# Optimization experiments

Measured on AMD Instinct MI355X. Metric: run time of the kernel, lower is better.

## Reference

```python
import jax, jax.numpy as jnp
import numpy as np

H, W, C = 96, 96, 21
SIGMA_RGB = 3.0   # bilateral spatial sdims (as called in the original code)
SIGMA_XY = 64.0   # gaussian spatial sdims
SCHAN = 255.0     # bilateral color std
COMPAT = 10.0     # Potts compatibility weight (same for both kernels)
N_ITERS = 5


def _gauss_kernel(feats):
    # feats: [N, D] -> K[i,j] = exp(-0.5 * ||f_i - f_j||^2)
    sq = jnp.sum(feats * feats, axis=-1)
    d2 = sq[:, None] + sq[None, :] - 2.0 * (feats @ feats.T)
    return jnp.exp(-0.5 * jnp.maximum(d2, 0.0))


def setup_inputs() -> dict:
    key = jax.random.key(0)
    k1, k2, k3 = jax.random.split(key, 3)
    logits = jax.random.normal(k1, (1, C, H, W), dtype=jnp.float32)
    labels = jax.random.randint(k2, (1, H, W), 0, C, dtype=jnp.int32)
    image = jax.random.uniform(k3, (1, 3, H, W), dtype=jnp.float32) * 255.0
    return {"logits": logits, "labels": labels, "image": image, "num_classes": C}


def reference(logits, labels, image, num_classes):
    # unary potentials: U = -log_softmax(logits)
    logp = jax.nn.log_softmax(logits, axis=1)              # [1,C,H,W]
    U = (-logp)[0].reshape(num_classes, -1).T              # [N,C]

    # pixel features
    yy, xx = jnp.meshgrid(jnp.arange(H), jnp.arange(W), indexing="ij")
    pos = jnp.stack([yy, xx], axis=-1).reshape(-1, 2).astype(logits.dtype)  # [N,2]
    rgb = image[0].transpose(1, 2, 0).reshape(-1, 3)        # [N,3]

    # dense pairwise kernels (exact Gaussian / bilateral, self-connection removed)
    N = H * W
    eye = jnp.eye(N, dtype=logits.dtype)
    Kg = _gauss_kernel(pos / SIGMA_XY) - eye
    fb = jnp.concatenate([pos / SIGMA_RGB, rgb / SCHAN], axis=-1)
    Kb = _gauss_kernel(fb) - eye

    # mean-field inference, Potts compatibility mu(l,l') = [l != l']
    Q0 = jax.nn.softmax(-U, axis=1)                         # [N,C]

    def step(Q, _):
        msg = Kg @ Q + Kb @ Q                               # [N,C] filtered Q
        pair = COMPAT * (jnp.sum(msg, axis=1, keepdims=True) - msg)
        Q = jax.nn.softmax(-U - pair, axis=1)
        return Q, None

    Q, _ = jax.lax.scan(step, Q0, None, length=N_ITERS)
    pairwise = Q.T.reshape(1, num_classes, H, W)

    # cross entropy (mean over pixels)
    ce = -jnp.mean(jnp.take_along_axis(logp, labels[:, None].astype(jnp.int32), axis=1))

    return ce + pairwise                                    # broadcast, as in original
```

## Files before the change

kernel.cpp:

```cpp
#include <hip/hip_runtime.h>
#include <hip/hip_fp16.h>

#define HH 96
#define WW 96
#define CC 21
#define NN (HH*WW)
#define NBLK (NN/256)
#define STRIDE 24
#define ROWF (WW*STRIDE)
#define QTROWS 24

typedef _Float16 f16x8 __attribute__((ext_vector_type(8)));
typedef float f32x4 __attribute__((ext_vector_type(4)));

union H8 { f16x8 v; __half2 h2[4]; };


__global__ __launch_bounds__(256) void k_setup(
    const float* __restrict__ logits, const int* __restrict__ labels,
    const float* __restrict__ image, float* __restrict__ U,
    float* __restrict__ Q0, _Float16* __restrict__ QTa,
    _Float16* __restrict__ QTb, float* __restrict__ gtab,
    float* __restrict__ partial) {
  const int t = threadIdx.x;
  const int i = blockIdx.x * 256 + t;

  float d[CC];
  float mx = -1e30f;
#pragma unroll
  for (int c = 0; c < CC; ++c) {
    d[c] = logits[c * NN + i];
    mx = fmaxf(mx, d[c]);
  }
  float s = 0.f;
#pragma unroll
  for (int c = 0; c < CC; ++c) { d[c] -= mx; s += __expf(d[c]); }
  const float lse = logf(s);
  const float inv = 1.f / s;
  const int lab = labels[i];
  float myU = 0.f;
#pragma unroll
  for (int c = 0; c < CC; ++c) {
    const float Uc = lse - d[c];
    const float q = __expf(d[c]) * inv;
    U[i * STRIDE + c] = Uc;
    Q0[i * STRIDE + c] = q;
    QTa[c * NN + i] = (_Float16)q;
    myU = (c == lab) ? Uc : myU;
  }
  const float rr = image[i] * (1.f / 255.f);
  const float rg = image[NN + i] * (1.f / 255.f);
  const float rb = image[2 * NN + i] * (1.f / 255.f);
  U[i * STRIDE + 21] = 0.f;
  U[i * STRIDE + 22] = 0.f;
  U[i * STRIDE + 23] = 0.f;
  Q0[i * STRIDE + 21] = rr;
  Q0[i * STRIDE + 22] = rg;
  Q0[i * STRIDE + 23] = rb;
  QTa[21 * NN + i] = (_Float16)rr;
  QTa[22 * NN + i] = (_Float16)rg;
  QTa[23 * NN + i] = (_Float16)rb;
  QTb[21 * NN + i] = (_Float16)rr;
  QTb[22 * NN + i] = (_Float16)rg;
  QTb[23 * NN + i] = (_Float16)rb;

  if (blockIdx.x == 0 && t < 96) {
    const float dv = (float)t * (1.f / 64.f);
    gtab[t] = __expf(-0.5f * dv * dv);
  }

  __shared__ float red[256];
  red[t] = myU;
  __syncthreads();
  for (int off = 128; off > 0; off >>= 1) {
    if (t < off) red[t] += red[t + off];
    __syncthreads();
  }
  if (t == 0) partial[blockIdx.x] = red[0];
}

__global__ __launch_bounds__(256) void k_gauss_y(
    const float* __restrict__ Qin, float* __restrict__ Gy,
    const float* __restrict__ gtab) {
  __shared__ float g[96];
  if (threadIdx.x < 96) g[threadIdx.x] = gtab[threadIdx.x];
  __syncthreads();
  const int idx = blockIdx.x * 256 + threadIdx.x;
  const int y = idx / ROWF;
  const int rem = idx - y * ROWF;
  const float* base = Qin + rem;
  float acc = 0.f;
#pragma unroll 8
  for (int yp = 0; yp < HH; ++yp)
    acc = fmaf(g[abs(y - yp)], base[yp * ROWF], acc);
  Gy[idx] = acc;
}

__global__ __launch_bounds__(256) void k_gauss_x(
    const float* __restrict__ Gy, float* __restrict__ G,
    const float* __restrict__ gtab) {
  __shared__ float g[96];
  if (threadIdx.x < 96) g[threadIdx.x] = gtab[threadIdx.x];
  __syncthreads();
  const int idx = blockIdx.x * 256 + threadIdx.x;
  const int y = idx / ROWF;
  const int rem = idx - y * ROWF;
  const int x = rem / STRIDE;
  const int c = rem - x * STRIDE;
  const float* base = Gy + y * ROWF + c;
  float acc = 0.f;
#pragma unroll 8
  for (int xp = 0; xp < WW; ++xp)
    acc = fmaf(g[abs(x - xp)], base[xp * STRIDE], acc);
  G[idx] = acc;
}

__global__ __launch_bounds__(512) void k_bilat(
    const float* __restrict__ U, const float* __restrict__ Qin,
    const float* __restrict__ G, const _Float16* __restrict__ QT,
    float* __restrict__ Qout, _Float16* __restrict__ QTout) {
  __shared__ __half sytab[64];
  __shared__ __half2 sxtab[64];
  __shared__ float psum[8][16][24];

  const int tid = threadIdx.x;
  const int w = tid >> 6;
  const int l = tid & 63;
  const int g = l >> 4;
  const int q = l & 15;

  if (tid < 64) {
    const float dv = (float)(tid - 32);
    sytab[tid] = __float2half(__expf(dv * dv * (-1.f / 18.f)));
    const float dv1 = dv + 1.f;
    sxtab[tid] = __floats2half2_rn(__expf(dv * dv * (-1.f / 18.f)),
                                   __expf(dv1 * dv1 * (-1.f / 18.f)));
  }
  __syncthreads();

  const int tile = blockIdx.x;
  const int ty0 = (tile / 24) * 4;
  const int tx0 = (tile - (tile / 24) * 24) * 4;

  const int pr = q >> 2, pc = q & 3;
  const int yi = ty0 + pr, xi = tx0 + pc;
  const int ipix = yi * WW + xi;

  const float4 rown = *(const float4*)(Qin + ipix * STRIDE + 20);
  const __half2 ri_r = __float2half2_rn(rown.y);
  const __half2 ri_g = __float2half2_rn(rown.z);
  const __half2 ri_b = __float2half2_rn(rown.w);
  const __half2 mhalf = __floats2half2_rn(-0.5f, -0.5f);
  const __half hzero = __float2half(0.f);

  const int xs = tx0 - 16;
  const int xbase0 = (xs > 0 ? xs : 0) & ~7;
  const int rows0 = (w < 4) ? w * 5 : 20 + (w - 4) * 4;
  const int nrun = ((w < 4) ? 5 : 4) * 5;
  const int nck = (nrun + 3) >> 2;

  const int brow2 = (16 + q > 23) ? 23 : 16 + q;

  f32x4 acc0 = {0.f, 0.f, 0.f, 0.f};
  f32x4 acc1 = {0.f, 0.f, 0.f, 0.f};

#pragma unroll 2
  for (int ck = 0; ck < 7; ++ck) {
    if (ck >= nck) break;
    const int r = ck * 4 + g;
    const int wr = r / 5;
    const int cs = r - wr * 5;
    const int yj = ty0 - 16 + rows0 + wr;
    const int xb = xbase0 + cs * 8;
    const bool ok = (r < nrun) & (yj >= 0) & (yj < HH) & (xb <= WW - 8);
    const int yc = min(max(yj, 0), HH - 1);
    const int xc = min(xb, WW - 8);
    const int jb = yc * WW + xc;

    H8 b1, b2, rj, gj, bj;
    b1.v = *(const f16x8*)(QT + q * NN + jb);
    b2.v = *(const f16x8*)(QT + brow2 * NN + jb);
    rj.v = *(const f16x8*)(QT + 21 * NN + jb);
    gj.v = *(const f16x8*)(QT + 22 * NN + jb);
    bj.v = *(const f16x8*)(QT + 23 * NN + jb);

    const int dy = yj - yi;
    const int iy = min(max(dy + 32, 0), 63);
    const __half syv = ok ? sytab[iy] : hzero;
    const __half2 sy2 = __half2half2(syv);
    const int dx0 = xb - xi;
    const int ix0 = min(max(dx0 + 32, 0), 57);

    H8 af;
#pragma unroll
    for (int e2 = 0; e2 < 4; ++e2) {
      const __half2 sx2 = sxtab[ix0 + 2 * e2];
      const __half2 dr = __hsub2(rj.h2[e2], ri_r);
      const __half2 dg = __hsub2(gj.h2[e2], ri_g);
      const __half2 db = __hsub2(bj.h2[e2], ri_b);
      __half2 d2c = __hmul2(dr, dr);
      d2c = __hfma2(dg, dg, d2c);
      d2c = __hfma2(db, db, d2c);
      const __half2 ec = h2exp(__hmul2(d2c, mhalf));
      af.h2[e2] = __hmul2(__hmul2(sy2, sx2), ec);
    }
    acc0 = __builtin_amdgcn_mfma_f32_16x16x32_f16(af.v, b1.v, acc0, 0, 0, 0);
    acc1 = __builtin_amdgcn_mfma_f32_16x16x32_f16(af.v, b2.v, acc1, 0, 0, 0);
  }

#pragma unroll
  for (int reg = 0; reg < 4; ++reg) {
    psum[w][g * 4 + reg][q] = acc0[reg];
    if (q < 8) psum[w][g * 4 + reg][16 + q] = acc1[reg];
  }
  __syncthreads();

  const int half_ = l >> 5;
  const int cl = l & 31;
  const bool act = cl < CC;
  const int pix = w * 2 + half_;
  const int ip = (ty0 + (pix >> 2)) * WW + tx0 + (pix & 3);
  float Qic = 0.f;
  if (cl < STRIDE) Qic = Qin[ip * STRIDE + cl];
  float tcv = 0.f, Uc = 0.f, Gc = 0.f;
  if (act) {
    tcv = psum[0][pix][cl] + psum[1][pix][cl] + psum[2][pix][cl] +
          psum[3][pix][cl] + psum[4][pix][cl] + psum[5][pix][cl] +
          psum[6][pix][cl] + psum[7][pix][cl];
    Uc = U[ip * STRIDE + cl];
    Gc = G[ip * STRIDE + cl];
  }
  const float contrib = act ? (tcv + Gc - 2.f * Qic) : 0.f;
  float tot = contrib;
#pragma unroll
  for (int off = 16; off >= 1; off >>= 1) tot += __shfl_xor(tot, off, 32);
  const float lc = act ? (-Uc - 10.f * (tot - contrib)) : -1e30f;
  float mxl = lc;
#pragma unroll
  for (int off = 16; off >= 1; off >>= 1)
    mxl = fmaxf(mxl, __shfl_xor(mxl, off, 32));
  const float e = act ? __expf(lc - mxl) : 0.f;
  float se = e;
#pragma unroll
  for (int off = 16; off >= 1; off >>= 1) se += __shfl_xor(se, off, 32);
  const float qnew = e / se;
  if (cl < STRIDE) Qout[ip * STRIDE + cl] = act ? qnew : Qic;
  if (act) QTout[cl * NN + ip] = (_Float16)qnew;
}

__global__ __launch_bounds__(256) void k_out(
    const float* __restrict__ Q, const float* __restrict__ partial,
    float* __restrict__ out) {
  __shared__ float ces;
  if (threadIdx.x < 64) {
    float v = (threadIdx.x < NBLK) ? partial[threadIdx.x] : 0.f;
#pragma unroll
    for (int off = 32; off > 0; off >>= 1) v += __shfl_down(v, off);
    if (threadIdx.x == 0) ces = v * (1.f / (float)NN);
  }
  __syncthreads();
  const int idx = blockIdx.x * 256 + threadIdx.x;
  if (idx >= CC * NN) return;
  const int c = idx / NN;
  const int i = idx - c * NN;
  out[idx] = ces + Q[i * STRIDE + c];
}

extern "C" void kernel_launch(void* const* d_in, const int* in_sizes, int n_in,
                              void* d_out, int out_size, void* d_ws,
                              size_t ws_size, hipStream_t stream) {
  const float* logits = (const float*)d_in[0];
  const int* labels = (const int*)d_in[1];
  const float* image = (const float*)d_in[2];
  float* ws = (float*)d_ws;

  float* U = ws;
  float* Qa = U + NN * STRIDE;
  float* Qb = Qa + NN * STRIDE;
  float* Gy = Qb + NN * STRIDE;
  float* G = Gy + NN * STRIDE;
  float* gtab = G + NN * STRIDE;
  float* partial = gtab + 96;
  float* cepad = partial + 64;
  _Float16* QTa = (_Float16*)(cepad + 64);
  _Float16* QTb = QTa + QTROWS * NN;

  k_setup<<<NBLK, 256, 0, stream>>>(logits, labels, image, U, Qa, QTa, QTb,
                                    gtab, partial);

  const float* qi = Qa;
  float* qo = Qb;
  const _Float16* qti = QTa;
  _Float16* qto = QTb;
  const int gblk = NN * STRIDE / 256;
  for (int it = 0; it < 5; ++it) {
    k_gauss_y<<<gblk, 256, 0, stream>>>(qi, Gy, gtab);
    k_gauss_x<<<gblk, 256, 0, stream>>>(Gy, G, gtab);
    k_bilat<<<576, 512, 0, stream>>>(U, qi, G, qti, qo, qto);
    qi = qo;
    qo = (qo == Qb) ? Qa : Qb;
    const _Float16* tmp = qti;
    qti = qto;
    qto = (_Float16*)tmp;
  }

  k_out<<<(CC * NN + 255) / 256, 256, 0, stream>>>(qi, partial, (float*)d_out);
}
```

Baseline: 156.8 us.

## Fuse Gaussian x-pass into bilateral kernel and tile QT into 8-pixel blocks

Removes the separate k_gauss_x launch per iteration. The bilateral kernel now computes the x-direction Gaussian sum itself from the y-filtered buffer during its epilogue, using a shared-memory copy of the Gaussian table. The transposed fp16 Q buffer is also relaid out so each 8-pixel run stores all 24 channels contiguously (192 halves), which makes the five per-step vector loads hit one contiguous region. The trade-off is a 96-tap serial loop per active thread in the bilateral epilogue, which lengthens that kernel's tail.

```diff
diff --git a/kernel.cpp b/kernel.cpp
--- a/kernel.cpp
+++ b/kernel.cpp
@@ -8,7 +8,7 @@
 #define NBLK (NN/256)
 #define STRIDE 24
 #define ROWF (WW*STRIDE)
-#define QTROWS 24
+#define NRUN (NN/8)
 
 typedef _Float16 f16x8 __attribute__((ext_vector_type(8)));
 typedef float f32x4 __attribute__((ext_vector_type(4)));
@@ -24,6 +24,7 @@
     float* __restrict__ partial) {
   const int t = threadIdx.x;
   const int i = blockIdx.x * 256 + t;
+  const int qoff = (i >> 3) * 192 + (i & 7);
 
   float d[CC];
   float mx = -1e30f;
@@ -45,7 +46,7 @@
     const float q = __expf(d[c]) * inv;
     U[i * STRIDE + c] = Uc;
     Q0[i * STRIDE + c] = q;
-    QTa[c * NN + i] = (_Float16)q;
+    QTa[qoff + c * 8] = (_Float16)q;
     myU = (c == lab) ? Uc : myU;
   }
   const float rr = image[i] * (1.f / 255.f);
@@ -57,12 +58,12 @@
   Q0[i * STRIDE + 21] = rr;
   Q0[i * STRIDE + 22] = rg;
   Q0[i * STRIDE + 23] = rb;
-  QTa[21 * NN + i] = (_Float16)rr;
-  QTa[22 * NN + i] = (_Float16)rg;
-  QTa[23 * NN + i] = (_Float16)rb;
-  QTb[21 * NN + i] = (_Float16)rr;
-  QTb[22 * NN + i] = (_Float16)rg;
-  QTb[23 * NN + i] = (_Float16)rb;
+  QTa[qoff + 21 * 8] = (_Float16)rr;
+  QTa[qoff + 22 * 8] = (_Float16)rg;
+  QTa[qoff + 23 * 8] = (_Float16)rb;
+  QTb[qoff + 21 * 8] = (_Float16)rr;
+  QTb[qoff + 22 * 8] = (_Float16)rg;
+  QTb[qoff + 23 * 8] = (_Float16)rb;
 
   if (blockIdx.x == 0 && t < 96) {
     const float dv = (float)t * (1.f / 64.f);
@@ -96,31 +97,14 @@
   Gy[idx] = acc;
 }
 
-__global__ __launch_bounds__(256) void k_gauss_x(
-    const float* __restrict__ Gy, float* __restrict__ G,
-    const float* __restrict__ gtab) {
-  __shared__ float g[96];
-  if (threadIdx.x < 96) g[threadIdx.x] = gtab[threadIdx.x];
-  __syncthreads();
-  const int idx = blockIdx.x * 256 + threadIdx.x;
-  const int y = idx / ROWF;
-  const int rem = idx - y * ROWF;
-  const int x = rem / STRIDE;
-  const int c = rem - x * STRIDE;
-  const float* base = Gy + y * ROWF + c;
-  float acc = 0.f;
-#pragma unroll 8
-  for (int xp = 0; xp < WW; ++xp)
-    acc = fmaf(g[abs(x - xp)], base[xp * STRIDE], acc);
-  G[idx] = acc;
-}
-
 __global__ __launch_bounds__(512) void k_bilat(
     const float* __restrict__ U, const float* __restrict__ Qin,
-    const float* __restrict__ G, const _Float16* __restrict__ QT,
-    float* __restrict__ Qout, _Float16* __restrict__ QTout) {
+    const float* __restrict__ Gy, const _Float16* __restrict__ QT,
+    const float* __restrict__ gtab, float* __restrict__ Qout,
+    _Float16* __restrict__ QTout) {
   __shared__ __half sytab[64];
   __shared__ __half2 sxtab[64];
+  __shared__ float sgt[96];
   __shared__ float psum[8][16][24];
 
   const int tid = threadIdx.x;
@@ -135,6 +119,8 @@
     const float dv1 = dv + 1.f;
     sxtab[tid] = __floats2half2_rn(__expf(dv * dv * (-1.f / 18.f)),
                                    __expf(dv1 * dv1 * (-1.f / 18.f)));
+  } else if (tid < 160) {
+    sgt[tid - 64] = gtab[tid - 64];
   }
   __syncthreads();
 
@@ -159,7 +145,7 @@
   const int nrun = ((w < 4) ? 5 : 4) * 5;
   const int nck = (nrun + 3) >> 2;
 
-  const int brow2 = (16 + q > 23) ? 23 : 16 + q;
+  const int row2 = (16 + q > 23) ? 23 : 16 + q;
 
   f32x4 acc0 = {0.f, 0.f, 0.f, 0.f};
   f32x4 acc1 = {0.f, 0.f, 0.f, 0.f};
@@ -175,14 +161,14 @@
     const bool ok = (r < nrun) & (yj >= 0) & (yj < HH) & (xb <= WW - 8);
     const int yc = min(max(yj, 0), HH - 1);
     const int xc = min(xb, WW - 8);
-    const int jb = yc * WW + xc;
+    const _Float16* base = QT + (yc * 12 + (xc >> 3)) * 192;
 
     H8 b1, b2, rj, gj, bj;
-    b1.v = *(const f16x8*)(QT + q * NN + jb);
-    b2.v = *(const f16x8*)(QT + brow2 * NN + jb);
-    rj.v = *(const f16x8*)(QT + 21 * NN + jb);
-    gj.v = *(const f16x8*)(QT + 22 * NN + jb);
-    bj.v = *(const f16x8*)(QT + 23 * NN + jb);
+    b1.v = *(const f16x8*)(base + q * 8);
+    b2.v = *(const f16x8*)(base + row2 * 8);
+    rj.v = *(const f16x8*)(base + 21 * 8);
+    gj.v = *(const f16x8*)(base + 22 * 8);
+    bj.v = *(const f16x8*)(base + 23 * 8);
 
     const int dy = yj - yi;
     const int iy = min(max(dy + 32, 0), 63);
@@ -219,7 +205,8 @@
   const int cl = l & 31;
   const bool act = cl < CC;
   const int pix = w * 2 + half_;
-  const int ip = (ty0 + (pix >> 2)) * WW + tx0 + (pix & 3);
+  const int py = ty0 + (pix >> 2), px = tx0 + (pix & 3);
+  const int ip = py * WW + px;
   float Qic = 0.f;
   if (cl < STRIDE) Qic = Qin[ip * STRIDE + cl];
   float tcv = 0.f, Uc = 0.f, Gc = 0.f;
@@ -228,7 +215,10 @@
           psum[3][pix][cl] + psum[4][pix][cl] + psum[5][pix][cl] +
           psum[6][pix][cl] + psum[7][pix][cl];
     Uc = U[ip * STRIDE + cl];
-    Gc = G[ip * STRIDE + cl];
+    const float* grow = Gy + py * ROWF + cl;
+#pragma unroll 8
+    for (int xp = 0; xp < WW; ++xp)
+      Gc = fmaf(sgt[abs(px - xp)], grow[xp * STRIDE], Gc);
   }
   const float contrib = act ? (tcv + Gc - 2.f * Qic) : 0.f;
   float tot = contrib;
@@ -245,7 +235,7 @@
   for (int off = 16; off >= 1; off >>= 1) se += __shfl_xor(se, off, 32);
   const float qnew = e / se;
   if (cl < STRIDE) Qout[ip * STRIDE + cl] = act ? qnew : Qic;
-  if (act) QTout[cl * NN + ip] = (_Float16)qnew;
+  if (act) QTout[(ip >> 3) * 192 + cl * 8 + (ip & 7)] = (_Float16)qnew;
 }
 
 __global__ __launch_bounds__(256) void k_out(
@@ -278,12 +268,11 @@
   float* Qa = U + NN * STRIDE;
   float* Qb = Qa + NN * STRIDE;
   float* Gy = Qb + NN * STRIDE;
-  float* G = Gy + NN * STRIDE;
-  float* gtab = G + NN * STRIDE;
+  float* gtab = Gy + NN * STRIDE;
   float* partial = gtab + 96;
   float* cepad = partial + 64;
   _Float16* QTa = (_Float16*)(cepad + 64);
-  _Float16* QTb = QTa + QTROWS * NN;
+  _Float16* QTb = QTa + NRUN * 192;
 
   k_setup<<<NBLK, 256, 0, stream>>>(logits, labels, image, U, Qa, QTa, QTb,
                                     gtab, partial);
@@ -295,8 +284,7 @@
   const int gblk = NN * STRIDE / 256;
   for (int it = 0; it < 5; ++it) {
     k_gauss_y<<<gblk, 256, 0, stream>>>(qi, Gy, gtab);
-    k_gauss_x<<<gblk, 256, 0, stream>>>(Gy, G, gtab);
-    k_bilat<<<576, 512, 0, stream>>>(U, qi, G, qti, qo, qto);
+    k_bilat<<<576, 512, 0, stream>>>(U, qi, Gy, qti, gtab, qo, qto);
     qi = qo;
     qo = (qo == Qb) ? Qa : Qb;
     const _Float16* tmp = qti;
```

Measured after the change: 142.6 us. -9.1%, faster.
